# Kernel optimization log

Measured on AMD Instinct MI355X. Metric: run time of the kernel, lower is better.

Reference implementation:

```python
import jax, jax.numpy as jnp
import numpy as np

B, A, G = 256, 64, 978          # batch, n_atoms, num_gene
D_DRUG, D_CELL, D_DOSE = 128, 50, 128
CELL_IN, DOSE_IN = 978, 12
GLOBAL = D_DRUG + D_CELL + D_DOSE   # 306
EXP_IN = GLOBAL + 128               # 434
E, TOP_K = 4, 2


def setup_inputs() -> dict:
    key = jax.random.key(0)
    ks = jax.random.split(key, 24)
    w = lambda k, s: jax.random.normal(k, s, jnp.float32) * 0.05
    return {
        "drug_atom_embed": jax.random.normal(ks[0], (B, A, D_DRUG), jnp.float32),
        "input_cell_gex": jax.random.normal(ks[1], (B, CELL_IN), jnp.float32),
        "input_pert_idose": jax.random.normal(ks[2], (B, DOSE_IN), jnp.float32),
        # LinearEncoder: 978 -> 200 -> 100 -> 50 (ReLU after each)
        "cell_W1": w(ks[3], (CELL_IN, 200)), "cell_b1": jnp.zeros((200,), jnp.float32),
        "cell_W2": w(ks[4], (200, 100)),     "cell_b2": jnp.zeros((100,), jnp.float32),
        "cell_W3": w(ks[5], (100, D_CELL)),  "cell_b3": jnp.zeros((D_CELL,), jnp.float32),
        # DoseEncoder: 12 -> 64 -> 128 (ReLU after each; dropout off at eval)
        "dose_W1": w(ks[6], (DOSE_IN, 64)),  "dose_b1": jnp.zeros((64,), jnp.float32),
        "dose_W2": w(ks[7], (64, D_DOSE)),   "dose_b2": jnp.zeros((D_DOSE,), jnp.float32),
        # gene index embedding [num_gene, 128]
        "gene_emb": w(ks[8], (G, 128)),
        # GatingNetwork: 306 -> 128 -> 4
        "gate_W1": w(ks[9], (GLOBAL, 128)),  "gate_b1": jnp.zeros((128,), jnp.float32),
        "gate_W2": w(ks[10], (128, E)),      "gate_b2": jnp.zeros((E,), jnp.float32),
        # 4 ExpertNetworks stacked: 434 -> 128 -> 1
        "exp_W1": w(ks[11], (E, EXP_IN, 128)), "exp_b1": jnp.zeros((E, 128), jnp.float32),
        "exp_W2": w(ks[12], (E, 128, 1)),      "exp_b2": jnp.zeros((E, 1), jnp.float32),
    }


def reference(drug_atom_embed, input_cell_gex, input_pert_idose,
              cell_W1, cell_b1, cell_W2, cell_b2, cell_W3, cell_b3,
              dose_W1, dose_b1, dose_W2, dose_b2, gene_emb,
              gate_W1, gate_b1, gate_W2, gate_b2,
              exp_W1, exp_b1, exp_W2, exp_b2):
    relu = jax.nn.relu
    # drug: sum atom embeddings -> [B, 128]
    drug = drug_atom_embed.sum(axis=1)
    # cell encoder -> [B, 50]
    cell = relu(input_cell_gex @ cell_W1 + cell_b1)
    cell = relu(cell @ cell_W2 + cell_b2)
    cell = relu(cell @ cell_W3 + cell_b3)
    # dose encoder -> [B, 128]
    dose = relu(input_pert_idose @ dose_W1 + dose_b1)
    dose = relu(dose @ dose_W2 + dose_b2)
    # global features [B, 306]
    g = jnp.concatenate([drug, cell, dose], axis=1)
    # gating: top-k sparse gates [B, E]
    logits = relu(g @ gate_W1 + gate_b1) @ gate_W2 + gate_b2
    top_v, top_i = jax.lax.top_k(logits, TOP_K)
    top_g = jax.nn.softmax(top_v, axis=1)
    gates = jnp.zeros_like(logits).at[jnp.arange(logits.shape[0])[:, None], top_i].set(top_g)
    # gene-aware expert input [B, G, 434]
    expert_input = jnp.concatenate([
        jnp.broadcast_to(g[:, None, :], (g.shape[0], G, GLOBAL)),
        jnp.broadcast_to(gene_emb[None, :, :], (g.shape[0], G, 128)),
    ], axis=2)
    # all experts: [B, E, G, 128] -> [B, E, G]
    h = relu(jnp.einsum('bgi,eih->begh', expert_input, exp_W1) + exp_b1[None, :, None, :])
    o = jnp.einsum('begh,eho->beg', h, exp_W2) + exp_b2[None, :, :1]  # exp_b2[e,0] broadcast
    predictions = jnp.einsum('beg,be->bg', o, gates)
    return predictions, cell
```

## Files before the change

kernel.cpp:

```cpp
#include <hip/hip_runtime.h>

#define NB 256
#define NA 64
#define NG 978
#define CELL_IN 978
#define DOSE_IN 12
#define GLOBAL_F 306
#define EXP_IN 434
#define NE 4

#define WS_SEL 0
#define WS_U   (WS_SEL + NB*4)
#define WS_V   (WS_U + NB*256)

#define AB_GRID (NB + 245)

__device__ __forceinline__ float wave_reduce(float p) {
    #pragma unroll
    for (int off = 32; off > 0; off >>= 1) p += __shfl_down(p, off, 64);
    return p;
}

__global__ __launch_bounds__(1024) void ab_kernel(
    const float* __restrict__ drug, const float* __restrict__ gex,
    const float* __restrict__ idose,
    const float* __restrict__ cW1, const float* __restrict__ cb1,
    const float* __restrict__ cW2, const float* __restrict__ cb2,
    const float* __restrict__ cW3, const float* __restrict__ cb3,
    const float* __restrict__ dW1, const float* __restrict__ db1,
    const float* __restrict__ dW2, const float* __restrict__ db2,
    const float* __restrict__ gW1, const float* __restrict__ gb1,
    const float* __restrict__ gW2, const float* __restrict__ gb2,
    const float* __restrict__ eW1, const float* __restrict__ eb1,
    const float* __restrict__ gene,
    float* __restrict__ ws, float* __restrict__ cell_out)
{
    __shared__ float s_gex[CELL_IN];
    __shared__ float s_g[GLOBAL_F];
    __shared__ float s_h1[200];
    __shared__ float s_h2[100];
    __shared__ float s_gh[128];
    __shared__ float s_d1[64];
    __shared__ int   s_isel[2];
    __shared__ float s_part[16 * 200];
    __shared__ float s_pu[32 * 128];
    __shared__ float s_ag[4][128];
    __shared__ float s_ap[4][8][128];

    const int blk = blockIdx.x, tid = threadIdx.x;

    if (blk >= NB) {
        const int gq = tid >> 8, lt = tid & 255;
        const int g = (blk - NB) * 4 + gq;
        if (lt < 128) s_ag[gq][lt] = (g < NG) ? gene[g * 128 + lt] : 0.f;
        __syncthreads();
        const int e = lt >> 6, ks = (lt >> 5) & 1, h4 = lt & 31;
        const float* wp = eW1 + ((size_t)e * EXP_IN + GLOBAL_F) * 128 + 4 * h4;
        float4 acc = {0.f, 0.f, 0.f, 0.f};
        const int k0 = ks * 64;
        #pragma unroll 8
        for (int k = k0; k < k0 + 64; ++k) {
            float4 w = *(const float4*)(wp + (size_t)k * 128);
            float x = s_ag[gq][k];
            acc.x += x * w.x; acc.y += x * w.y; acc.z += x * w.z; acc.w += x * w.w;
        }
        *(float4*)(&s_ap[gq][e * 2 + ks][4 * h4]) = acc;
        __syncthreads();
        if (lt < 128 && g < NG) {
            int oe = lt >> 5, oh4 = lt & 31;
            float4 p0 = *(const float4*)(&s_ap[gq][oe * 2 + 0][4 * oh4]);
            float4 p1 = *(const float4*)(&s_ap[gq][oe * 2 + 1][4 * oh4]);
            float4 o = {p0.x + p1.x, p0.y + p1.y, p0.z + p1.z, p0.w + p1.w};
            *(float4*)(ws + WS_V + (size_t)g * 512 + oe * 128 + 4 * oh4) = o;
        }
        return;
    }

    const int b = blk;

    if (tid < CELL_IN) s_gex[tid] = gex[b * CELL_IN + tid];
    {
        int row = tid >> 7, d = tid & 127;
        const float* p = drug + ((size_t)b * NA) * 128 + d;
        float acc = 0.f;
        #pragma unroll
        for (int i = 0; i < 8; ++i) acc += p[(size_t)(i * 8 + row) * 128];
        s_pu[row * 128 + d] = acc;
    }
    __syncthreads();
    if (tid < 128) {
        float a = 0.f;
        #pragma unroll
        for (int r = 0; r < 8; ++r) a += s_pu[r * 128 + tid];
        s_g[tid] = a;
    } else if (tid < 192) {
        int j = tid - 128;
        float acc = db1[j];
        #pragma unroll
        for (int i = 0; i < DOSE_IN; ++i)
            acc += idose[b * DOSE_IN + i] * dW1[i * 64 + j];
        s_d1[j] = fmaxf(acc, 0.f);
    }
    __syncthreads();
    if (tid < 128) {
        float acc = db2[tid];
        #pragma unroll 8
        for (int i = 0; i < 64; ++i) acc += s_d1[i] * dW2[i * 128 + tid];
        s_g[178 + tid] = fmaxf(acc, 0.f);
    }
    __syncthreads();

    {
        int q = tid & 63, ks = tid >> 6;
        if (q < 50) {
            int i0 = ks * 62, i1 = min(i0 + 62, CELL_IN);
            float4 acc = {0.f, 0.f, 0.f, 0.f};
            #pragma unroll 4
            for (int i = i0; i < i1; ++i) {
                float4 w = *(const float4*)(cW1 + (size_t)i * 200 + 4 * q);
                float x = s_gex[i];
                acc.x += x * w.x; acc.y += x * w.y; acc.z += x * w.z; acc.w += x * w.w;
            }
            *(float4*)(&s_part[ks * 200 + 4 * q]) = acc;
        }
    }
    __syncthreads();
    if (tid < 200) {
        float a = cb1[tid];
        #pragma unroll
        for (int ks = 0; ks < 16; ++ks) a += s_part[ks * 200 + tid];
        s_h1[tid] = fmaxf(a, 0.f);
    }
    __syncthreads();

    {
        int q = tid & 31, ks = tid >> 5;
        if (q < 25 && ks < 16) {
            int i0 = ks * 13, i1 = min(i0 + 13, 200);
            float4 acc = {0.f, 0.f, 0.f, 0.f};
            #pragma unroll
            for (int i = i0; i < i1; ++i) {
                float4 w = *(const float4*)(cW2 + (size_t)i * 100 + 4 * q);
                float x = s_h1[i];
                acc.x += x * w.x; acc.y += x * w.y; acc.z += x * w.z; acc.w += x * w.w;
            }
            *(float4*)(&s_part[ks * 100 + 4 * q]) = acc;
        }
    }
    __syncthreads();
    if (tid < 100) {
        float a = cb2[tid];
        #pragma unroll
        for (int ks = 0; ks < 16; ++ks) a += s_part[ks * 100 + tid];
        s_h2[tid] = fmaxf(a, 0.f);
    }
    __syncthreads();

    {
        int j = tid & 63, ks = tid >> 6;
        if (j < 50 && ks < 8) {
            int i0 = ks * 13, i1 = min(i0 + 13, 100);
            float acc = 0.f;
            #pragma unroll
            for (int i = i0; i < i1; ++i) acc += s_h2[i] * cW3[i * 50 + j];
            s_part[ks * 64 + j] = acc;
        }
    }
    __syncthreads();
    if (tid < 50) {
        float a = cb3[tid];
        #pragma unroll
        for (int ks = 0; ks < 8; ++ks) a += s_part[ks * 64 + tid];
        float r = fmaxf(a, 0.f);
        s_g[128 + tid] = r;
        cell_out[b * 50 + tid] = r;
    }
    __syncthreads();

    {
        int q = tid & 31, ks = tid >> 5;
        if (ks < 16) {
            int i0 = ks * 20, i1 = min(i0 + 20, GLOBAL_F);
            float4 acc = {0.f, 0.f, 0.f, 0.f};
            #pragma unroll
            for (int i = i0; i < i1; ++i) {
                float4 w = *(const float4*)(gW1 + (size_t)i * 128 + 4 * q);
                float x = s_g[i];
                acc.x += x * w.x; acc.y += x * w.y; acc.z += x * w.z; acc.w += x * w.w;
            }
            *(float4*)(&s_part[ks * 128 + 4 * q]) = acc;
        }
    }
    __syncthreads();
    if (tid < 128) {
        float a = gb1[tid];
        #pragma unroll
        for (int ks = 0; ks < 16; ++ks) a += s_part[ks * 128 + tid];
        s_gh[tid] = fmaxf(a, 0.f);
    }
    __syncthreads();

    if (tid < 64) {
        float h0 = s_gh[tid], h1 = s_gh[tid + 64];
        float logit[NE];
        #pragma unroll
        for (int j = 0; j < NE; ++j) {
            float p = h0 * gW2[tid * NE + j] + h1 * gW2[(tid + 64) * NE + j];
            p = wave_reduce(p);
            logit[j] = p + gb2[j];
        }
        if (tid == 0) {
            int i1 = 0; float v1 = logit[0];
            #pragma unroll
            for (int i = 1; i < NE; ++i) if (logit[i] > v1) { v1 = logit[i]; i1 = i; }
            int i2 = -1; float v2 = -__builtin_inff();
            #pragma unroll
            for (int i = 0; i < NE; ++i) {
                if (i == i1) continue;
                if (logit[i] > v2) { v2 = logit[i]; i2 = i; }
            }
            float ex = __expf(v2 - v1);
            float inv = 1.f / (1.f + ex);
            s_isel[0] = i1; s_isel[1] = i2;
            ws[WS_SEL + b * 4 + 0] = (float)i1;
            ws[WS_SEL + b * 4 + 1] = (float)i2;
            ws[WS_SEL + b * 4 + 2] = inv;
            ws[WS_SEL + b * 4 + 3] = ex * inv;
        }
    }
    __syncthreads();

    {
        int es = tid >> 9, ks = (tid >> 5) & 15, h4 = tid & 31;
        int e = s_isel[es];
        int i0 = ks * 20, i1 = min(i0 + 20, GLOBAL_F);
        const float* wp = eW1 + (size_t)e * EXP_IN * 128 + 4 * h4;
        float4 acc = {0.f, 0.f, 0.f, 0.f};
        #pragma unroll
        for (int i = i0; i < i1; ++i) {
            float4 w = *(const float4*)(wp + (size_t)i * 128);
            float x = s_g[i];
            acc.x += x * w.x; acc.y += x * w.y; acc.z += x * w.z; acc.w += x * w.w;
        }
        *(float4*)(&s_pu[(es * 16 + ks) * 128 + 4 * h4]) = acc;
    }
    __syncthreads();
    if (tid < 256) {
        int es = tid >> 7, h = tid & 127;
        int e = s_isel[es];
        float a = eb1[e * 128 + h];
        #pragma unroll
        for (int ks = 0; ks < 16; ++ks) a += s_pu[(es * 16 + ks) * 128 + h];
        ws[WS_U + (size_t)b * 256 + es * 128 + h] = a;
    }
}

__global__ __launch_bounds__(256) void c_kernel(
    const float* __restrict__ eW2, const float* __restrict__ eb2,
    const float* __restrict__ ws, float* __restrict__ pred)
{
    __shared__ float s_u[256];
    __shared__ float s_w2[256];
    const int b = blockIdx.x >> 2, qt = blockIdx.x & 3, tid = threadIdx.x;

    const int ea = (int)ws[WS_SEL + b * 4 + 0];
    const int eb = (int)ws[WS_SEL + b * 4 + 1];
    const float gA = ws[WS_SEL + b * 4 + 2];
    const float gB = ws[WS_SEL + b * 4 + 3];
    const float bA = eb2[ea], bB = eb2[eb];

    s_u[tid] = ws[WS_U + (size_t)b * 256 + tid];
    s_w2[tid] = (tid < 128) ? eW2[ea * 128 + tid] : eW2[eb * 128 + (tid - 128)];
    __syncthreads();

    const int g = qt * 256 + tid;
    if (g < NG) {
        const float4* vA = (const float4*)(ws + WS_V + (size_t)g * 512 + ea * 128);
        const float4* vB = (const float4*)(ws + WS_V + (size_t)g * 512 + eb * 128);
        float dA = 0.f, dB = 0.f;
        #pragma unroll 8
        for (int k = 0; k < 32; ++k) {
            float4 va = vA[k], vb = vB[k];
            dA += fmaxf(s_u[4*k+0] + va.x, 0.f) * s_w2[4*k+0]
                + fmaxf(s_u[4*k+1] + va.y, 0.f) * s_w2[4*k+1]
                + fmaxf(s_u[4*k+2] + va.z, 0.f) * s_w2[4*k+2]
                + fmaxf(s_u[4*k+3] + va.w, 0.f) * s_w2[4*k+3];
            dB += fmaxf(s_u[128+4*k+0] + vb.x, 0.f) * s_w2[128+4*k+0]
                + fmaxf(s_u[128+4*k+1] + vb.y, 0.f) * s_w2[128+4*k+1]
                + fmaxf(s_u[128+4*k+2] + vb.z, 0.f) * s_w2[128+4*k+2]
                + fmaxf(s_u[128+4*k+3] + vb.w, 0.f) * s_w2[128+4*k+3];
        }
        pred[(size_t)b * NG + g] = gA * (dA + bA) + gB * (dB + bB);
    }
}

extern "C" void kernel_launch(void* const* d_in, const int* in_sizes, int n_in,
                              void* d_out, int out_size, void* d_ws, size_t ws_size,
                              hipStream_t stream) {
    const float* drug  = (const float*)d_in[0];
    const float* gex   = (const float*)d_in[1];
    const float* idose = (const float*)d_in[2];
    const float* cW1 = (const float*)d_in[3];  const float* cb1 = (const float*)d_in[4];
    const float* cW2 = (const float*)d_in[5];  const float* cb2 = (const float*)d_in[6];
    const float* cW3 = (const float*)d_in[7];  const float* cb3 = (const float*)d_in[8];
    const float* dW1 = (const float*)d_in[9];  const float* db1 = (const float*)d_in[10];
    const float* dW2 = (const float*)d_in[11]; const float* db2 = (const float*)d_in[12];
    const float* gene = (const float*)d_in[13];
    const float* gW1 = (const float*)d_in[14]; const float* gb1 = (const float*)d_in[15];
    const float* gW2 = (const float*)d_in[16]; const float* gb2 = (const float*)d_in[17];
    const float* eW1 = (const float*)d_in[18]; const float* eb1 = (const float*)d_in[19];
    const float* eW2 = (const float*)d_in[20]; const float* eb2 = (const float*)d_in[21];

    float* ws   = (float*)d_ws;
    float* out  = (float*)d_out;
    float* pred = out;
    float* cell = out + NB * NG;

    ab_kernel<<<AB_GRID, 1024, 0, stream>>>(drug, gex, idose,
        cW1, cb1, cW2, cb2, cW3, cb3, dW1, db1, dW2, db2,
        gW1, gb1, gW2, gb2, eW1, eb1, gene, ws, cell);
    c_kernel<<<NB * 4, 256, 0, stream>>>(eW2, eb2, ws, pred);
}
```

Before: 184.2 us.

## Tile gene projection by 64-gene blocks per expert and transpose V layout

The gene-embedding projection now runs as 64 blocks, each covering a 64-gene tile for one expert. Gene rows are staged in padded shared memory and each thread computes 8 hidden outputs, so eW1 rows are reused across 64 genes. V is stored gene-minor (tile, expert, hidden, gene), so the consumer kernel's per-lane loads coalesce across genes instead of each thread reading 512 contiguous floats. Shared memory is merged into one aliased buffer, and the cell layer-1 loop gets two independent accumulator chains to expose more ILP. Tail genes are zero-padded and still computed, and the consumer reads V padded to 16 tiles, which the workspace must be large enough to hold.

```diff
diff --git a/kernel.cpp b/kernel.cpp
--- a/kernel.cpp
+++ b/kernel.cpp
@@ -13,7 +13,18 @@
 #define WS_U   (WS_SEL + NB*4)
 #define WS_V   (WS_U + NB*256)
 
-#define AB_GRID (NB + 245)
+#define A_BLOCKS 64
+#define AB_GRID  (NB + A_BLOCKS)
+
+#define SM_PART 0
+#define SM_PU   3200
+#define SM_GEX  7296
+#define SM_G    8274
+#define SM_H1   8580
+#define SM_H2   8780
+#define SM_GH   8880
+#define SM_D1   9008
+#define SM_SIZE 9072
 
 __device__ __forceinline__ float wave_reduce(float p) {
     #pragma unroll
@@ -35,48 +46,51 @@
     const float* __restrict__ gene,
     float* __restrict__ ws, float* __restrict__ cell_out)
 {
-    __shared__ float s_gex[CELL_IN];
-    __shared__ float s_g[GLOBAL_F];
-    __shared__ float s_h1[200];
-    __shared__ float s_h2[100];
-    __shared__ float s_gh[128];
-    __shared__ float s_d1[64];
+    __shared__ float smem[SM_SIZE];
     __shared__ int   s_isel[2];
-    __shared__ float s_part[16 * 200];
-    __shared__ float s_pu[32 * 128];
-    __shared__ float s_ag[4][128];
-    __shared__ float s_ap[4][8][128];
 
     const int blk = blockIdx.x, tid = threadIdx.x;
 
     if (blk >= NB) {
-        const int gq = tid >> 8, lt = tid & 255;
-        const int g = (blk - NB) * 4 + gq;
-        if (lt < 128) s_ag[gq][lt] = (g < NG) ? gene[g * 128 + lt] : 0.f;
+        const int ablk = blk - NB;
+        const int tile = ablk >> 2, e = ablk & 3;
+        float* s_gene = smem;
+
+        for (int i = tid; i < 64 * 128; i += 1024) {
+            int gl = i >> 7, k = i & 127;
+            int g = tile * 64 + gl;
+            s_gene[gl * 129 + k] = (g < NG) ? gene[g * 128 + k] : 0.f;
+        }
         __syncthreads();
-        const int e = lt >> 6, ks = (lt >> 5) & 1, h4 = lt & 31;
-        const float* wp = eW1 + ((size_t)e * EXP_IN + GLOBAL_F) * 128 + 4 * h4;
-        float4 acc = {0.f, 0.f, 0.f, 0.f};
-        const int k0 = ks * 64;
-        #pragma unroll 8
-        for (int k = k0; k < k0 + 64; ++k) {
-            float4 w = *(const float4*)(wp + (size_t)k * 128);
-            float x = s_ag[gq][k];
-            acc.x += x * w.x; acc.y += x * w.y; acc.z += x * w.z; acc.w += x * w.w;
-        }
-        *(float4*)(&s_ap[gq][e * 2 + ks][4 * h4]) = acc;
-        __syncthreads();
-        if (lt < 128 && g < NG) {
-            int oe = lt >> 5, oh4 = lt & 31;
-            float4 p0 = *(const float4*)(&s_ap[gq][oe * 2 + 0][4 * oh4]);
-            float4 p1 = *(const float4*)(&s_ap[gq][oe * 2 + 1][4 * oh4]);
-            float4 o = {p0.x + p1.x, p0.y + p1.y, p0.z + p1.z, p0.w + p1.w};
-            *(float4*)(ws + WS_V + (size_t)g * 512 + oe * 128 + 4 * oh4) = o;
-        }
+
+        const int h16 = tid >> 6, g_in = tid & 63;
+        const float* wbase = eW1 + ((size_t)e * EXP_IN + GLOBAL_F) * 128 + h16 * 8;
+        float acc[8] = {};
+        #pragma unroll 4
+        for (int k = 0; k < 128; ++k) {
+            float x = s_gene[g_in * 129 + k];
+            float4 w0 = *(const float4*)(wbase + (size_t)k * 128);
+            float4 w1 = *(const float4*)(wbase + (size_t)k * 128 + 4);
+            acc[0] += x * w0.x; acc[1] += x * w0.y;
+            acc[2] += x * w0.z; acc[3] += x * w0.w;
+            acc[4] += x * w1.x; acc[5] += x * w1.y;
+            acc[6] += x * w1.z; acc[7] += x * w1.w;
+        }
+        float* vout = ws + WS_V + ((size_t)tile * 512 + e * 128 + h16 * 8) * 64 + g_in;
+        #pragma unroll
+        for (int j = 0; j < 8; ++j) vout[(size_t)j * 64] = acc[j];
         return;
     }
 
     const int b = blk;
+    float* s_part = smem + SM_PART;
+    float* s_pu   = smem + SM_PU;
+    float* s_gex  = smem + SM_GEX;
+    float* s_g    = smem + SM_G;
+    float* s_h1   = smem + SM_H1;
+    float* s_h2   = smem + SM_H2;
+    float* s_gh   = smem + SM_GH;
+    float* s_d1   = smem + SM_D1;
 
     if (tid < CELL_IN) s_gex[tid] = gex[b * CELL_IN + tid];
     {
@@ -114,14 +128,25 @@
         int q = tid & 63, ks = tid >> 6;
         if (q < 50) {
             int i0 = ks * 62, i1 = min(i0 + 62, CELL_IN);
-            float4 acc = {0.f, 0.f, 0.f, 0.f};
+            int n = i1 - i0, h2 = n >> 1;
+            float4 a0 = {0.f, 0.f, 0.f, 0.f}, a1 = {0.f, 0.f, 0.f, 0.f};
             #pragma unroll 4
-            for (int i = i0; i < i1; ++i) {
-                float4 w = *(const float4*)(cW1 + (size_t)i * 200 + 4 * q);
-                float x = s_gex[i];
-                acc.x += x * w.x; acc.y += x * w.y; acc.z += x * w.z; acc.w += x * w.w;
-            }
-            *(float4*)(&s_part[ks * 200 + 4 * q]) = acc;
+            for (int t = 0; t < h2; ++t) {
+                int ia = i0 + t, ib = i0 + h2 + t;
+                float4 wa = *(const float4*)(cW1 + (size_t)ia * 200 + 4 * q);
+                float4 wb = *(const float4*)(cW1 + (size_t)ib * 200 + 4 * q);
+                float xa = s_gex[ia], xb = s_gex[ib];
+                a0.x += xa * wa.x; a0.y += xa * wa.y; a0.z += xa * wa.z; a0.w += xa * wa.w;
+                a1.x += xb * wb.x; a1.y += xb * wb.y; a1.z += xb * wb.z; a1.w += xb * wb.w;
+            }
+            if (n & 1) {
+                int ia = i1 - 1;
+                float4 wa = *(const float4*)(cW1 + (size_t)ia * 200 + 4 * q);
+                float xa = s_gex[ia];
+                a0.x += xa * wa.x; a0.y += xa * wa.y; a0.z += xa * wa.z; a0.w += xa * wa.w;
+            }
+            float4 s = {a0.x + a1.x, a0.y + a1.y, a0.z + a1.z, a0.w + a1.w};
+            *(float4*)(&s_part[ks * 200 + 4 * q]) = s;
         }
     }
     __syncthreads();
@@ -261,7 +286,7 @@
 {
     __shared__ float s_u[256];
     __shared__ float s_w2[256];
-    const int b = blockIdx.x >> 2, qt = blockIdx.x & 3, tid = threadIdx.x;
+    const int b = blockIdx.x >> 2, quad = blockIdx.x & 3, tid = threadIdx.x;
 
     const int ea = (int)ws[WS_SEL + b * 4 + 0];
     const int eb = (int)ws[WS_SEL + b * 4 + 1];
@@ -273,25 +298,19 @@
     s_w2[tid] = (tid < 128) ? eW2[ea * 128 + tid] : eW2[eb * 128 + (tid - 128)];
     __syncthreads();
 
-    const int g = qt * 256 + tid;
-    if (g < NG) {
-        const float4* vA = (const float4*)(ws + WS_V + (size_t)g * 512 + ea * 128);
-        const float4* vB = (const float4*)(ws + WS_V + (size_t)g * 512 + eb * 128);
-        float dA = 0.f, dB = 0.f;
-        #pragma unroll 8
-        for (int k = 0; k < 32; ++k) {
-            float4 va = vA[k], vb = vB[k];
-            dA += fmaxf(s_u[4*k+0] + va.x, 0.f) * s_w2[4*k+0]
-                + fmaxf(s_u[4*k+1] + va.y, 0.f) * s_w2[4*k+1]
-                + fmaxf(s_u[4*k+2] + va.z, 0.f) * s_w2[4*k+2]
-                + fmaxf(s_u[4*k+3] + va.w, 0.f) * s_w2[4*k+3];
-            dB += fmaxf(s_u[128+4*k+0] + vb.x, 0.f) * s_w2[128+4*k+0]
-                + fmaxf(s_u[128+4*k+1] + vb.y, 0.f) * s_w2[128+4*k+1]
-                + fmaxf(s_u[128+4*k+2] + vb.z, 0.f) * s_w2[128+4*k+2]
-                + fmaxf(s_u[128+4*k+3] + vb.w, 0.f) * s_w2[128+4*k+3];
-        }
-        pred[(size_t)b * NG + g] = gA * (dA + bA) + gB * (dB + bB);
-    }
+    const int wv = tid >> 6, lane = tid & 63;
+    const int tile = quad * 4 + wv;
+    const float* vA = ws + WS_V + ((size_t)tile * 512 + ea * 128) * 64 + lane;
+    const float* vB = ws + WS_V + ((size_t)tile * 512 + eb * 128) * 64 + lane;
+
+    float dA = 0.f, dB = 0.f;
+    #pragma unroll 8
+    for (int h = 0; h < 128; ++h) {
+        dA += fmaxf(s_u[h]       + vA[(size_t)h * 64], 0.f) * s_w2[h];
+        dB += fmaxf(s_u[128 + h] + vB[(size_t)h * 64], 0.f) * s_w2[128 + h];
+    }
+    const int g = tile * 64 + lane;
+    if (g < NG) pred[(size_t)b * NG + g] = gA * (dA + bA) + gB * (dB + bB);
 }
 
 extern "C" void kernel_launch(void* const* d_in, const int* in_sizes, int n_in,
```

Measured after the change: 180.1 us. 2.2% less time.
